# Kernel tuning notes

Hardware: AMD Instinct MI355X
Metric: run time of the kernel (lower is better)

## Reference

```python
import jax, jax.numpy as jnp
import numpy as np

EPS = 1e-7  # keras backend epsilon
ROUTINGS = 3


def squash(x, axis=-1):
    s2 = jnp.sum(jnp.square(x), axis=axis, keepdims=True)
    scale = s2 / (1.0 + s2) / jnp.sqrt(s2 + EPS)
    return scale * x


def setup_inputs() -> dict:
    key = jax.random.key(0)
    k1, k2 = jax.random.split(key)
    B, In, in_dim = 64, 2048, 16
    N, D = 32, 32
    inputs = jax.random.normal(k1, (B, In, in_dim), dtype=jnp.float32)
    W = jax.random.normal(k2, (N, In, D, in_dim), dtype=jnp.float32)  # stddev=1.0 init per module
    return {"inputs": inputs, "W": W}


def reference(inputs, W):
    # inputs: [B, In, in_dim]; W: [N, In, D, in_dim]
    # u_hat[b,n,i,d] = sum_k W[n,i,d,k] * inputs[b,i,k]
    u_hat = jnp.einsum('nidk,bik->bnid', W, inputs)  # [B, N, In, D]
    B, N, In, D = u_hat.shape
    b = jnp.zeros((B, N, In), dtype=u_hat.dtype)
    v = None
    for _ in range(ROUTINGS):
        c = jax.nn.softmax(b, axis=1)                 # softmax over output capsules
        s = jnp.einsum('bni,bnid->bnd', c, u_hat)     # weighted sum over input capsules
        v = squash(s)                                 # [B, N, D]
        b = b + jnp.einsum('bnid,bnd->bni', u_hat, v) # agreement
    return v
```

## Files before the change

### kernel.cpp

```cpp
#include <hip/hip_runtime.h>


#define INP 2048
#define BB 64
#define KK 16
#define NN 32
#define DD 32
#define ICH 16
#define NCHUNK (INP / ICH)

typedef __attribute__((ext_vector_type(8))) short short8;
typedef __attribute__((ext_vector_type(16))) float f32x16;

__device__ __forceinline__ short bf_trunc(float f) {
  return (short)(__builtin_bit_cast(unsigned, f) >> 16);
}
__device__ __forceinline__ unsigned short bf_round(float f) {
  unsigned u = __builtin_bit_cast(unsigned, f);
  return (unsigned short)((u + 0x8000u) >> 16);
}
__device__ __forceinline__ float bf2f(unsigned short u) {
  return __builtin_bit_cast(float, (unsigned)u << 16);
}

__device__ __forceinline__ void split8(float4 w0, float4 w1, short8& h, short8& l) {
  float f[8] = {w0.x, w0.y, w0.z, w0.w, w1.x, w1.y, w1.z, w1.w};
#pragma unroll
  for (int j = 0; j < 8; ++j) {
    unsigned u = __builtin_bit_cast(unsigned, f[j]);
    h[j] = (short)(u >> 16);
    float hf = __builtin_bit_cast(float, u & 0xFFFF0000u);
    l[j] = bf_trunc(f[j] - hf);
  }
}

__device__ __forceinline__ short8 round8(float4 w0, float4 w1) {
  float f[8] = {w0.x, w0.y, w0.z, w0.w, w1.x, w1.y, w1.z, w1.w};
  short8 r;
#pragma unroll
  for (int j = 0; j < 8; ++j) r[j] = (short)bf_round(f[j]);
  return r;
}

__global__ __launch_bounds__(256) void kT(const float* __restrict__ x,
                                          short* __restrict__ xh,
                                          short* __restrict__ xl) {
  const int t = blockIdx.x * 256 + threadIdx.x;
  const int i = t >> 6, b = t & 63;
  const float4* xs = (const float4*)(x + ((size_t)b * INP + i) * KK);
  short8* dh = (short8*)(xh + ((size_t)i * BB + b) * KK);
  short8* dl = (short8*)(xl + ((size_t)i * BB + b) * KK);
#pragma unroll
  for (int h = 0; h < 2; ++h) {
    short8 hh, ll;
    split8(xs[h * 2], xs[h * 2 + 1], hh, ll);
    dh[h] = hh;
    dl[h] = ll;
  }
}

__global__ __launch_bounds__(256) void kS1c(const float* __restrict__ W,
                                            const short* __restrict__ xh,
                                            const short* __restrict__ xl,
                                            short* __restrict__ Wb,
                                            unsigned short* __restrict__ spart) {
  const int wv = threadIdx.x >> 6;
  const int lane = threadIdx.x & 63;
  const int bl = lane & 31;
  const int hi = lane >> 5;
  const int w = blockIdx.x * 4 + wv;
  const int n = w >> 7;
  const int ch = w & (NCHUNK - 1);

  f32x16 s0 = {};
  f32x16 s1 = {};

  const size_t fragoff = (((size_t)n * INP + (size_t)ch * ICH) * DD + bl) * KK + hi * 8;
  const float* Wp = W + fragoff;
  short* Wbp = Wb + fragoff;
  const short* xhp = xh + (size_t)ch * ICH * BB * KK + hi * 8;
  const short* xlp = xl + (size_t)ch * ICH * BB * KK + hi * 8;

#pragma unroll 2
  for (int ii = 0; ii < ICH; ++ii) {
    float4 w0 = *(const float4*)(Wp + (size_t)ii * (DD * KK));
    float4 w1 = *(const float4*)(Wp + (size_t)ii * (DD * KK) + 4);
    short8 whi, wlo;
    split8(w0, w1, whi, wlo);
    *(short8*)(Wbp + (size_t)ii * (DD * KK)) = round8(w0, w1);
    const short8 x0h = *(const short8*)(xhp + ii * (BB * KK) + bl * KK);
    const short8 x0l = *(const short8*)(xlp + ii * (BB * KK) + bl * KK);
    const short8 x1h = *(const short8*)(xhp + ii * (BB * KK) + (bl + 32) * KK);
    const short8 x1l = *(const short8*)(xlp + ii * (BB * KK) + (bl + 32) * KK);
    s0 = __builtin_amdgcn_mfma_f32_32x32x16_bf16(whi, x0h, s0, 0, 0, 0);
    s0 = __builtin_amdgcn_mfma_f32_32x32x16_bf16(whi, x0l, s0, 0, 0, 0);
    s0 = __builtin_amdgcn_mfma_f32_32x32x16_bf16(wlo, x0h, s0, 0, 0, 0);
    s1 = __builtin_amdgcn_mfma_f32_32x32x16_bf16(whi, x1h, s1, 0, 0, 0);
    s1 = __builtin_amdgcn_mfma_f32_32x32x16_bf16(whi, x1l, s1, 0, 0, 0);
    s1 = __builtin_amdgcn_mfma_f32_32x32x16_bf16(wlo, x1h, s1, 0, 0, 0);
  }

  const size_t off = ((size_t)ch * NN + n) * (DD * BB);
#pragma unroll
  for (int r = 0; r < 16; ++r) {
    const int d = (r & 3) + 8 * (r >> 2) + 4 * hi;
    spart[off + d * BB + bl] = bf_round(0.03125f * s0[r]);
    spart[off + d * BB + bl + 32] = bf_round(0.03125f * s1[r]);
  }
}

__global__ __launch_bounds__(256) void kA(const short* __restrict__ Wb,
                                          const short* __restrict__ xh,
                                          const short* __restrict__ xl,
                                          const float* __restrict__ vsum,
                                          unsigned short* __restrict__ ct) {
  const int wv = threadIdx.x >> 6;
  const int lane = threadIdx.x & 63;
  const int bl = lane & 31;
  const int hi = lane >> 5;
  const int w = blockIdx.x * 4 + wv;
  const int n = w >> 7;
  const int ch = w & (NCHUNK - 1);

  float vr0[16], vr1[16];
#pragma unroll
  for (int r = 0; r < 16; ++r) {
    const int d = (r & 3) + 8 * (r >> 2) + 4 * hi;
    vr0[r] = vsum[((size_t)n * DD + d) * BB + bl];
    vr1[r] = vsum[((size_t)n * DD + d) * BB + bl + 32];
  }

  const short* Wp = Wb + (((size_t)n * INP + (size_t)ch * ICH) * DD + bl) * KK + hi * 8;
  const short* xhp = xh + (size_t)ch * ICH * BB * KK + hi * 8;
  const short* xlp = xl + (size_t)ch * ICH * BB * KK + hi * 8;

#pragma unroll 2
  for (int ii = 0; ii < ICH; ++ii) {
    const short8 whi = *(const short8*)(Wp + (size_t)ii * (DD * KK));
    const short8 x0h = *(const short8*)(xhp + ii * (BB * KK) + bl * KK);
    const short8 x0l = *(const short8*)(xlp + ii * (BB * KK) + bl * KK);
    const short8 x1h = *(const short8*)(xhp + ii * (BB * KK) + (bl + 32) * KK);
    const short8 x1l = *(const short8*)(xlp + ii * (BB * KK) + (bl + 32) * KK);

    f32x16 u0 = {};
    u0 = __builtin_amdgcn_mfma_f32_32x32x16_bf16(whi, x0h, u0, 0, 0, 0);
    u0 = __builtin_amdgcn_mfma_f32_32x32x16_bf16(whi, x0l, u0, 0, 0, 0);
    f32x16 u1 = {};
    u1 = __builtin_amdgcn_mfma_f32_32x32x16_bf16(whi, x1h, u1, 0, 0, 0);
    u1 = __builtin_amdgcn_mfma_f32_32x32x16_bf16(whi, x1l, u1, 0, 0, 0);

    float p0 = 0.f, p1 = 0.f;
#pragma unroll
    for (int r = 0; r < 16; ++r) {
      p0 += u0[r] * vr0[r];
      p1 += u1[r] * vr1[r];
    }
    p0 += __shfl_xor(p0, 32, 64);
    p1 += __shfl_xor(p1, 32, 64);
    const int i = ch * ICH + ii;
    ct[((size_t)i * NN + n) * BB + lane] = bf_round((lane < 32) ? p0 : p1);
  }
}

__global__ __launch_bounds__(256) void kSM(unsigned short* __restrict__ ct) {
  const int wv = threadIdx.x >> 6;
  const int lane = threadIdx.x & 63;
  const int i = blockIdx.x * 4 + wv;
  unsigned short* p = ct + (size_t)i * NN * BB + lane;
  float a[NN];
  float m = -1e30f;
#pragma unroll
  for (int n = 0; n < NN; ++n) {
    a[n] = bf2f(p[n * BB]);
    m = fmaxf(m, a[n]);
  }
  float s = 0.f;
#pragma unroll
  for (int n = 0; n < NN; ++n) {
    a[n] = __expf(a[n] - m);
    s += a[n];
  }
  const float inv = 1.f / s;
#pragma unroll
  for (int n = 0; n < NN; ++n) p[n * BB] = bf_round(a[n] * inv);
}

__global__ __launch_bounds__(256) void kS(const short* __restrict__ Wb,
                                          const short* __restrict__ xh,
                                          const short* __restrict__ xl,
                                          const unsigned short* __restrict__ ct,
                                          unsigned short* __restrict__ spart) {
  const int wv = threadIdx.x >> 6;
  const int lane = threadIdx.x & 63;
  const int bl = lane & 31;
  const int hi = lane >> 5;
  const int w = blockIdx.x * 4 + wv;
  const int n = w >> 7;
  const int ch = w & (NCHUNK - 1);

  f32x16 s0 = {};
  f32x16 s1 = {};

  const short* Wp = Wb + (((size_t)n * INP + (size_t)ch * ICH) * DD + bl) * KK + hi * 8;
  const short* xhp = xh + (size_t)ch * ICH * BB * KK + hi * 8;
  const short* xlp = xl + (size_t)ch * ICH * BB * KK + hi * 8;

#pragma unroll 2
  for (int ii = 0; ii < ICH; ++ii) {
    const short8 whi = *(const short8*)(Wp + (size_t)ii * (DD * KK));
    const short8 x0h = *(const short8*)(xhp + ii * (BB * KK) + bl * KK);
    const short8 x0l = *(const short8*)(xlp + ii * (BB * KK) + bl * KK);
    const short8 x1h = *(const short8*)(xhp + ii * (BB * KK) + (bl + 32) * KK);
    const short8 x1l = *(const short8*)(xlp + ii * (BB * KK) + (bl + 32) * KK);

    f32x16 u0 = {};
    u0 = __builtin_amdgcn_mfma_f32_32x32x16_bf16(whi, x0h, u0, 0, 0, 0);
    u0 = __builtin_amdgcn_mfma_f32_32x32x16_bf16(whi, x0l, u0, 0, 0, 0);
    f32x16 u1 = {};
    u1 = __builtin_amdgcn_mfma_f32_32x32x16_bf16(whi, x1h, u1, 0, 0, 0);
    u1 = __builtin_amdgcn_mfma_f32_32x32x16_bf16(whi, x1l, u1, 0, 0, 0);

    const int i = ch * ICH + ii;
    const float c0 = bf2f(ct[((size_t)i * NN + n) * BB + bl]);
    const float c1 = bf2f(ct[((size_t)i * NN + n) * BB + bl + 32]);
#pragma unroll
    for (int r = 0; r < 16; ++r) {
      s0[r] += c0 * u0[r];
      s1[r] += c1 * u1[r];
    }
  }

  const size_t off = ((size_t)ch * NN + n) * (DD * BB);
#pragma unroll
  for (int r = 0; r < 16; ++r) {
    const int d = (r & 3) + 8 * (r >> 2) + 4 * hi;
    spart[off + d * BB + bl] = bf_round(s0[r]);
    spart[off + d * BB + bl + 32] = bf_round(s1[r]);
  }
}

__global__ void kR1h(const unsigned* __restrict__ spart, float2* __restrict__ st) {
  const int t = blockIdx.x * 128 + threadIdx.x;
  float s0 = 0.f, s1 = 0.f;
  for (int ch = 0; ch < NCHUNK; ++ch) {
    const unsigned u = spart[(size_t)ch * (NN * DD * BB / 2) + t];
    s0 += bf2f((unsigned short)(u & 0xFFFFu));
    s1 += bf2f((unsigned short)(u >> 16));
  }
  st[t] = make_float2(s0, s1);
}

__global__ void kR2(const float* __restrict__ st, float* __restrict__ vsum,
                    float* __restrict__ out, int first, int last) {
  const int t = blockIdx.x * 256 + threadIdx.x;
  const int b = t & 63;
  const int n = t >> 6;
  float sd[DD];
  float s2 = 0.f;
#pragma unroll
  for (int d = 0; d < DD; ++d) {
    sd[d] = st[(n * DD + d) * BB + b];
    s2 += sd[d] * sd[d];
  }
  const float scale = s2 / (1.f + s2) / sqrtf(s2 + 1e-7f);
#pragma unroll
  for (int d = 0; d < DD; ++d) {
    const float v = scale * sd[d];
    const size_t idx = (size_t)(n * DD + d) * BB + b;
    vsum[idx] = first ? v : (vsum[idx] + v);
    if (last) out[((size_t)b * NN + n) * DD + d] = v;
  }
}

extern "C" void kernel_launch(void* const* d_in, const int* in_sizes, int n_in,
                              void* d_out, int out_size, void* d_ws,
                              size_t ws_size, hipStream_t stream) {
  const float* x = (const float*)d_in[0];
  const float* W = (const float*)d_in[1];
  float* out = (float*)d_out;

  short* xh = (short*)d_ws;
  short* xl = xh + (size_t)INP * BB * KK;
  short* Wbuf = xl + (size_t)INP * BB * KK;
  unsigned short* ct = (unsigned short*)(Wbuf + (size_t)NN * INP * DD * KK);
  unsigned short* sparth = ct + (size_t)INP * NN * BB;
  float* st = (float*)(sparth + (size_t)NCHUNK * NN * DD * BB);
  float* vsum = st + (size_t)NN * DD * BB;

  const int gW = (NN * NCHUNK) / 4;
  const int gT = (INP * BB) / 256;
  const int gSM = INP / 4;
  const int gR1h = (NN * DD * BB / 2) / 128;
  const int gR2 = (BB * NN) / 256;

  kT<<<gT, 256, 0, stream>>>(x, xh, xl);

  kS1c<<<gW, 256, 0, stream>>>(W, xh, xl, Wbuf, sparth);
  kR1h<<<gR1h, 128, 0, stream>>>((const unsigned*)sparth, (float2*)st);
  kR2<<<gR2, 256, 0, stream>>>(st, vsum, out, 1, 0);
  for (int it = 1; it < 3; ++it) {
    kA<<<gW, 256, 0, stream>>>(Wbuf, xh, xl, vsum, ct);
    kSM<<<gSM, 256, 0, stream>>>(ct);
    kS<<<gW, 256, 0, stream>>>(Wbuf, xh, xl, ct, sparth);
    kR1h<<<gR1h, 128, 0, stream>>>((const unsigned*)sparth, (float2*)st);
    kR2<<<gR2, 256, 0, stream>>>(st, vsum, out, 0, it == 2);
  }
}
```

Measured before the change: 185.7 us.

## Split W bf16 conversion into separate kernel, cut precision in agreement, resize squash launch

Moves the fp32-to-bf16 rounding of W into a standalone grid-stride kernel. The first routing pass now reuses kS with a uniform coupling constant instead of the three-term split-precision kS1c, so the first s uses only rounded W. The agreement kernel drops the low-part x MFMA, halving its matrix work at some accuracy cost. The squash kernel launches with 64-thread blocks to spread its small workload over more CUs.

Measured after the change: 216.7 us. 16.7% more time.

```diff
diff --git a/kernel.cpp b/kernel.cpp
--- a/kernel.cpp
+++ b/kernel.cpp
@@ -40,6 +40,16 @@
 #pragma unroll
   for (int j = 0; j < 8; ++j) r[j] = (short)bf_round(f[j]);
   return r;
+}
+
+__global__ __launch_bounds__(256) void kWc(const float* __restrict__ W,
+                                           short* __restrict__ Wb) {
+  const size_t stride = (size_t)gridDim.x * 256;
+  const size_t nch = (size_t)NN * INP * DD * KK / 8;
+  const float4* W4 = (const float4*)W;
+  short8* Wb8 = (short8*)Wb;
+  for (size_t t = (size_t)blockIdx.x * 256 + threadIdx.x; t < nch; t += stride)
+    Wb8[t] = round8(W4[2 * t], W4[2 * t + 1]);
 }
 
 __global__ __launch_bounds__(256) void kT(const float* __restrict__ x,
@@ -59,59 +69,8 @@
   }
 }
 
-__global__ __launch_bounds__(256) void kS1c(const float* __restrict__ W,
-                                            const short* __restrict__ xh,
-                                            const short* __restrict__ xl,
-                                            short* __restrict__ Wb,
-                                            unsigned short* __restrict__ spart) {
-  const int wv = threadIdx.x >> 6;
-  const int lane = threadIdx.x & 63;
-  const int bl = lane & 31;
-  const int hi = lane >> 5;
-  const int w = blockIdx.x * 4 + wv;
-  const int n = w >> 7;
-  const int ch = w & (NCHUNK - 1);
-
-  f32x16 s0 = {};
-  f32x16 s1 = {};
-
-  const size_t fragoff = (((size_t)n * INP + (size_t)ch * ICH) * DD + bl) * KK + hi * 8;
-  const float* Wp = W + fragoff;
-  short* Wbp = Wb + fragoff;
-  const short* xhp = xh + (size_t)ch * ICH * BB * KK + hi * 8;
-  const short* xlp = xl + (size_t)ch * ICH * BB * KK + hi * 8;
-
-#pragma unroll 2
-  for (int ii = 0; ii < ICH; ++ii) {
-    float4 w0 = *(const float4*)(Wp + (size_t)ii * (DD * KK));
-    float4 w1 = *(const float4*)(Wp + (size_t)ii * (DD * KK) + 4);
-    short8 whi, wlo;
-    split8(w0, w1, whi, wlo);
-    *(short8*)(Wbp + (size_t)ii * (DD * KK)) = round8(w0, w1);
-    const short8 x0h = *(const short8*)(xhp + ii * (BB * KK) + bl * KK);
-    const short8 x0l = *(const short8*)(xlp + ii * (BB * KK) + bl * KK);
-    const short8 x1h = *(const short8*)(xhp + ii * (BB * KK) + (bl + 32) * KK);
-    const short8 x1l = *(const short8*)(xlp + ii * (BB * KK) + (bl + 32) * KK);
-    s0 = __builtin_amdgcn_mfma_f32_32x32x16_bf16(whi, x0h, s0, 0, 0, 0);
-    s0 = __builtin_amdgcn_mfma_f32_32x32x16_bf16(whi, x0l, s0, 0, 0, 0);
-    s0 = __builtin_amdgcn_mfma_f32_32x32x16_bf16(wlo, x0h, s0, 0, 0, 0);
-    s1 = __builtin_amdgcn_mfma_f32_32x32x16_bf16(whi, x1h, s1, 0, 0, 0);
-    s1 = __builtin_amdgcn_mfma_f32_32x32x16_bf16(whi, x1l, s1, 0, 0, 0);
-    s1 = __builtin_amdgcn_mfma_f32_32x32x16_bf16(wlo, x1h, s1, 0, 0, 0);
-  }
-
-  const size_t off = ((size_t)ch * NN + n) * (DD * BB);
-#pragma unroll
-  for (int r = 0; r < 16; ++r) {
-    const int d = (r & 3) + 8 * (r >> 2) + 4 * hi;
-    spart[off + d * BB + bl] = bf_round(0.03125f * s0[r]);
-    spart[off + d * BB + bl + 32] = bf_round(0.03125f * s1[r]);
-  }
-}
-
 __global__ __launch_bounds__(256) void kA(const short* __restrict__ Wb,
                                           const short* __restrict__ xh,
-                                          const short* __restrict__ xl,
                                           const float* __restrict__ vsum,
                                           unsigned short* __restrict__ ct) {
   const int wv = threadIdx.x >> 6;
@@ -132,22 +91,17 @@
 
   const short* Wp = Wb + (((size_t)n * INP + (size_t)ch * ICH) * DD + bl) * KK + hi * 8;
   const short* xhp = xh + (size_t)ch * ICH * BB * KK + hi * 8;
-  const short* xlp = xl + (size_t)ch * ICH * BB * KK + hi * 8;
 
 #pragma unroll 2
   for (int ii = 0; ii < ICH; ++ii) {
     const short8 whi = *(const short8*)(Wp + (size_t)ii * (DD * KK));
     const short8 x0h = *(const short8*)(xhp + ii * (BB * KK) + bl * KK);
-    const short8 x0l = *(const short8*)(xlp + ii * (BB * KK) + bl * KK);
     const short8 x1h = *(const short8*)(xhp + ii * (BB * KK) + (bl + 32) * KK);
-    const short8 x1l = *(const short8*)(xlp + ii * (BB * KK) + (bl + 32) * KK);
 
     f32x16 u0 = {};
     u0 = __builtin_amdgcn_mfma_f32_32x32x16_bf16(whi, x0h, u0, 0, 0, 0);
-    u0 = __builtin_amdgcn_mfma_f32_32x32x16_bf16(whi, x0l, u0, 0, 0, 0);
     f32x16 u1 = {};
     u1 = __builtin_amdgcn_mfma_f32_32x32x16_bf16(whi, x1h, u1, 0, 0, 0);
-    u1 = __builtin_amdgcn_mfma_f32_32x32x16_bf16(whi, x1l, u1, 0, 0, 0);
 
     float p0 = 0.f, p1 = 0.f;
 #pragma unroll
@@ -189,7 +143,8 @@
                                           const short* __restrict__ xh,
                                           const short* __restrict__ xl,
                                           const unsigned short* __restrict__ ct,
-                                          unsigned short* __restrict__ spart) {
+                                          unsigned short* __restrict__ spart,
+                                          int uniform_c) {
   const int wv = threadIdx.x >> 6;
   const int lane = threadIdx.x & 63;
   const int bl = lane & 31;
@@ -220,9 +175,15 @@
     u1 = __builtin_amdgcn_mfma_f32_32x32x16_bf16(whi, x1h, u1, 0, 0, 0);
     u1 = __builtin_amdgcn_mfma_f32_32x32x16_bf16(whi, x1l, u1, 0, 0, 0);
 
-    const int i = ch * ICH + ii;
-    const float c0 = bf2f(ct[((size_t)i * NN + n) * BB + bl]);
-    const float c1 = bf2f(ct[((size_t)i * NN + n) * BB + bl + 32]);
+    float c0, c1;
+    if (uniform_c) {
+      c0 = 0.03125f;
+      c1 = 0.03125f;
+    } else {
+      const int i = ch * ICH + ii;
+      c0 = bf2f(ct[((size_t)i * NN + n) * BB + bl]);
+      c1 = bf2f(ct[((size_t)i * NN + n) * BB + bl + 32]);
+    }
 #pragma unroll
     for (int r = 0; r < 16; ++r) {
       s0[r] += c0 * u0[r];
@@ -252,7 +213,7 @@
 
 __global__ void kR2(const float* __restrict__ st, float* __restrict__ vsum,
                     float* __restrict__ out, int first, int last) {
-  const int t = blockIdx.x * 256 + threadIdx.x;
+  const int t = blockIdx.x * 64 + threadIdx.x;
   const int b = t & 63;
   const int n = t >> 6;
   float sd[DD];
@@ -291,18 +252,19 @@
   const int gT = (INP * BB) / 256;
   const int gSM = INP / 4;
   const int gR1h = (NN * DD * BB / 2) / 128;
-  const int gR2 = (BB * NN) / 256;
-
+  const int gR2 = (BB * NN) / 64;
+
+  kWc<<<2048, 256, 0, stream>>>(W, Wbuf);
   kT<<<gT, 256, 0, stream>>>(x, xh, xl);
 
-  kS1c<<<gW, 256, 0, stream>>>(W, xh, xl, Wbuf, sparth);
+  kS<<<gW, 256, 0, stream>>>(Wbuf, xh, xl, (const unsigned short*)nullptr, sparth, 1);
   kR1h<<<gR1h, 128, 0, stream>>>((const unsigned*)sparth, (float2*)st);
-  kR2<<<gR2, 256, 0, stream>>>(st, vsum, out, 1, 0);
+  kR2<<<gR2, 64, 0, stream>>>(st, vsum, out, 1, 0);
   for (int it = 1; it < 3; ++it) {
-    kA<<<gW, 256, 0, stream>>>(Wbuf, xh, xl, vsum, ct);
+    kA<<<gW, 256, 0, stream>>>(Wbuf, xh, vsum, ct);
     kSM<<<gSM, 256, 0, stream>>>(ct);
-    kS<<<gW, 256, 0, stream>>>(Wbuf, xh, xl, ct, sparth);
+    kS<<<gW, 256, 0, stream>>>(Wbuf, xh, xl, ct, sparth, 0);
     kR1h<<<gR1h, 128, 0, stream>>>((const unsigned*)sparth, (float2*)st);
-    kR2<<<gR2, 256, 0, stream>>>(st, vsum, out, 0, it == 2);
-  }
-}
+    kR2<<<gR2, 64, 0, stream>>>(st, vsum, out, 0, it == 2);
+  }
+}
```
